# Performance work log

Measured on AMD Instinct MI355X. Metric: run time of the kernel, lower is better.

## Reference

```python
import jax, jax.numpy as jnp
import numpy as np

N = 100000
E = 1600000
F_IN, F_HID, F_OUT = 128, 32, 2


def setup_inputs() -> dict:
    key = jax.random.key(0)
    k1, k2, k3, k4 = jax.random.split(key, 4)
    x = jax.random.normal(k1, (N, F_IN), dtype=jnp.float32)
    edge_index = jax.random.randint(k2, (2, E), 0, N, dtype=jnp.int64)
    # Glorot-style init like torch_geometric GCNConv
    W1 = jax.random.normal(k3, (F_IN, F_HID), dtype=jnp.float32) * (1.0 / np.sqrt(F_IN))
    b1 = jnp.zeros((F_HID,), dtype=jnp.float32)
    W2 = jax.random.normal(k4, (F_HID, F_OUT), dtype=jnp.float32) * (1.0 / np.sqrt(F_HID))
    b2 = jnp.zeros((F_OUT,), dtype=jnp.float32)
    return {"x": x, "edge_index": edge_index, "W1": W1, "b1": b1, "W2": W2, "b2": b2}


def _gcn_conv(x, row, col, norm, W, b):
    # GCNConv: transform, then normalized aggregate (source -> target), then bias
    h = x @ W                                   # [N, F_out]
    msg = norm[:, None] * h[row]                # gather + scale, [E+N, F_out]
    out = jax.ops.segment_sum(msg, col, num_segments=N)  # scatter-add to targets
    return out + b


def reference(x, edge_index, W1, b1, W2, b2):
    # add self-loops (GCNConv default)
    loops = jnp.arange(N, dtype=edge_index.dtype)
    row = jnp.concatenate([edge_index[0], loops])
    col = jnp.concatenate([edge_index[1], loops])
    # symmetric normalization: deg^{-1/2}[row] * deg^{-1/2}[col], deg = in-degree w/ self-loops
    deg = jax.ops.segment_sum(jnp.ones_like(col, dtype=x.dtype), col, num_segments=N)
    dinv = jnp.where(deg > 0, jax.lax.rsqrt(deg), 0.0)
    norm = dinv[row] * dinv[col]                # [E+N]

    h = _gcn_conv(x, row, col, norm, W1, b1)
    h = jax.nn.relu(h)
    h = _gcn_conv(h, row, col, norm, W2, b2)
    return jax.nn.log_softmax(h, axis=1)
```

## Files before the change

kernel.cpp:

```cpp
#include <hip/hip_runtime.h>
#include <hip/hip_bf16.h>
#include <math.h>
#include <stdint.h>


#define GNN_N 100000
#define GNN_E 1600000
#define NBUCK 391
#define CAP 4608
#define CHB 4096

typedef float fx2 __attribute__((ext_vector_type(2)));
typedef short short8x __attribute__((ext_vector_type(8)));
typedef float f32x4 __attribute__((ext_vector_type(4)));

__device__ inline uint16_t bf16_bits(float f) {
    uint32_t u = __float_as_uint(f);
    return (uint16_t)((u + 0x7fffu + ((u >> 16) & 1u)) >> 16);
}

__global__ __launch_bounds__(256) void k_bucket(const int* __restrict__ row,
                                                const int* __restrict__ col,
                                                int* __restrict__ bucket_fill,
                                                uint32_t* __restrict__ slab, int e) {
    __shared__ int hist[NBUCK];
    __shared__ int base[NBUCK];
    const int tid = threadIdx.x;
    const int e0 = blockIdx.x * CHB;
    const int m = min(CHB, e - e0);
    const bool full = (m == CHB);

    for (int i = tid; i < NBUCK; i += 256) hist[i] = 0;

    int cc[16], rr[16], pp[16];
    if (full) {
        const int4* c4 = (const int4*)(col + e0);
        const int4* r4 = (const int4*)(row + e0);
        #pragma unroll
        for (int t = 0; t < 4; ++t) {
            int4 c = c4[tid + t * 256];
            int4 r = r4[tid + t * 256];
            cc[t * 4 + 0] = c.x; cc[t * 4 + 1] = c.y;
            cc[t * 4 + 2] = c.z; cc[t * 4 + 3] = c.w;
            rr[t * 4 + 0] = r.x; rr[t * 4 + 1] = r.y;
            rr[t * 4 + 2] = r.z; rr[t * 4 + 3] = r.w;
        }
        __syncthreads();
        #pragma unroll
        for (int t = 0; t < 16; ++t)
            pp[t] = atomicAdd(&hist[cc[t] >> 8], 1);
    } else {
        __syncthreads();
        #pragma unroll
        for (int t = 0; t < 16; ++t) {
            int i = tid + t * 256;
            if (i < m) {
                cc[t] = col[e0 + i];
                rr[t] = row[e0 + i];
                pp[t] = atomicAdd(&hist[cc[t] >> 8], 1);
            }
        }
    }
    __syncthreads();
    for (int i = tid; i < NBUCK; i += 256) {
        int bb = (i + blockIdx.x * 131) % NBUCK;
        base[bb] = atomicAdd(&bucket_fill[bb], hist[bb]);
    }
    __syncthreads();
    if (full) {
        #pragma unroll
        for (int t = 0; t < 16; ++t) {
            int b = cc[t] >> 8;
            int p = base[b] + pp[t];
            if (p < CAP)
                slab[(size_t)b * CAP + p] = ((uint32_t)rr[t] << 8) | (uint32_t)(cc[t] & 255);
        }
    } else {
        #pragma unroll
        for (int t = 0; t < 16; ++t) {
            int i = tid + t * 256;
            if (i < m) {
                int b = cc[t] >> 8;
                int p = base[b] + pp[t];
                if (p < CAP)
                    slab[(size_t)b * CAP + p] = ((uint32_t)rr[t] << 8) | (uint32_t)(cc[t] & 255);
            }
        }
    }
}

__global__ __launch_bounds__(512) void k_fine(const uint32_t* __restrict__ slab,
                                              const int* __restrict__ bucket_fill,
                                              int* __restrict__ sorted_row,
                                              int* __restrict__ offsets,
                                              float* __restrict__ dinv, int n) {
    __shared__ int hist[256];
    __shared__ int excl[256];
    __shared__ int wsum[4];
    __shared__ int s_gbase;
    __shared__ uint32_t stage[CAP];
    const int tid = threadIdx.x;
    const int b0 = blockIdx.x * 2;
    const int lane = tid & 63, wave = tid >> 6;

    if (blockIdx.x == gridDim.x - 1 && tid == 511) offsets[n] = GNN_E;

    if (tid < 64) {
        int s = 0;
        for (int i = tid; i < b0; i += 64) s += bucket_fill[i];
        #pragma unroll
        for (int m = 32; m >= 1; m >>= 1) s += __shfl_xor(s, m);
        if (tid == 0) s_gbase = s;
    }
    __syncthreads();
    int gbase = s_gbase;

    for (int pass = 0; pass < 2; ++pass) {
        const int b = b0 + pass;
        if (b >= NBUCK) break;
        const int nb = min(bucket_fill[b], CAP);
        const uint32_t* sl = slab + (size_t)b * CAP;

        if (tid < 256) hist[tid] = 0;
        __syncthreads();
        uint32_t uu[9];
        int pp[9];
        #pragma unroll
        for (int j = 0; j < 9; ++j) {
            int i = tid + j * 512;
            if (i < nb) {
                uint32_t u = sl[i];
                uu[j] = u;
                pp[j] = atomicAdd(&hist[u & 255u], 1);
            }
        }
        __syncthreads();
        int v = 0, inc = 0;
        if (tid < 256) {
            v = hist[tid];
            inc = v;
            #pragma unroll
            for (int d = 1; d < 64; d <<= 1) {
                int t = __shfl_up(inc, d);
                if (lane >= d) inc += t;
            }
            if (lane == 63) wsum[wave] = inc;
        }
        __syncthreads();
        if (tid == 0) {
            int a = 0;
            #pragma unroll
            for (int w = 0; w < 4; ++w) { int t = wsum[w]; wsum[w] = a; a += t; }
        }
        __syncthreads();
        if (tid < 256) {
            int ex = inc - v + wsum[wave];
            excl[tid] = ex;
            int c = b * 256 + tid;
            if (c < n) {
                offsets[c] = gbase + ex;
                dinv[c] = rsqrtf((float)(v + 1));
            }
        }
        __syncthreads();
        #pragma unroll
        for (int j = 0; j < 9; ++j) {
            int i = tid + j * 512;
            if (i < nb)
                stage[excl[uu[j] & 255u] + pp[j]] = uu[j] >> 8;
        }
        __syncthreads();
        for (int i = tid; i < nb; i += 512)
            sorted_row[gbase + i] = (int)stage[i];
        gbase += nb;
        __syncthreads();
    }
}

#define XPAD 136
__global__ __launch_bounds__(256) void k_matmul1(const float* __restrict__ x,
                                                 const float* __restrict__ W1,
                                                 const float* __restrict__ dinv,
                                                 uint32_t* __restrict__ h1q, int n) {
    __shared__ uint16_t xs[64 * XPAD];
    __shared__ uint16_t w1t[32 * XPAD];
    const int tid = threadIdx.x;
    const int nodeBase = blockIdx.x * 64;

    for (int i = tid; i < 4096; i += 256) {
        int k = i >> 5, c = i & 31;
        w1t[c * XPAD + k] = bf16_bits(W1[i]);
    }
    {
        const float4* x4 = (const float4*)x;
        for (int i = tid; i < 64 * 32; i += 256) {
            int node = i >> 5;
            int k4 = i & 31;
            float4 v = make_float4(0.f, 0.f, 0.f, 0.f);
            if (nodeBase + node < n)
                v = x4[(size_t)(nodeBase + node) * 32 + k4];
            int b = node * XPAD + k4 * 4;
            xs[b + 0] = bf16_bits(v.x); xs[b + 1] = bf16_bits(v.y);
            xs[b + 2] = bf16_bits(v.z); xs[b + 3] = bf16_bits(v.w);
        }
    }
    __syncthreads();

    const int wave = tid >> 6;
    const int lane = tid & 63;
    const int nn = lane & 15;
    const int quad = lane >> 4;
    f32x4 acc0 = {0.f, 0.f, 0.f, 0.f};
    f32x4 acc1 = {0.f, 0.f, 0.f, 0.f};
    const int xrow = (wave * 16 + nn) * XPAD;
    #pragma unroll
    for (int s = 0; s < 4; ++s) {
        const int kof = s * 32 + quad * 8;
        short8x bfrag = *(const short8x*)&xs[xrow + kof];
        short8x a0 = *(const short8x*)&w1t[nn * XPAD + kof];
        short8x a1 = *(const short8x*)&w1t[(16 + nn) * XPAD + kof];
        acc0 = __builtin_amdgcn_mfma_f32_16x16x32_bf16(a0, bfrag, acc0, 0, 0, 0);
        acc1 = __builtin_amdgcn_mfma_f32_16x16x32_bf16(a1, bfrag, acc1, 0, 0, 0);
    }
    const int gn = nodeBase + wave * 16 + nn;
    if (gn < n) {
        float d = dinv[gn];
        int w0 = 0, w1 = 0;
        w0 = __builtin_amdgcn_cvt_pk_fp8_f32(acc0[0] * d, acc0[1] * d, w0, false);
        w0 = __builtin_amdgcn_cvt_pk_fp8_f32(acc0[2] * d, acc0[3] * d, w0, true);
        w1 = __builtin_amdgcn_cvt_pk_fp8_f32(acc1[0] * d, acc1[1] * d, w1, false);
        w1 = __builtin_amdgcn_cvt_pk_fp8_f32(acc1[2] * d, acc1[3] * d, w1, true);
        h1q[(size_t)gn * 8 + quad] = (uint32_t)w0;
        h1q[(size_t)gn * 8 + 4 + quad] = (uint32_t)w1;
    }
}

__device__ inline void fp8x16_acc(float* a, uint4 u) {
    fx2 p;
    p = __builtin_amdgcn_cvt_pk_f32_fp8(u.x, false); a[0] += p.x;  a[1] += p.y;
    p = __builtin_amdgcn_cvt_pk_f32_fp8(u.x, true);  a[2] += p.x;  a[3] += p.y;
    p = __builtin_amdgcn_cvt_pk_f32_fp8(u.y, false); a[4] += p.x;  a[5] += p.y;
    p = __builtin_amdgcn_cvt_pk_f32_fp8(u.y, true);  a[6] += p.x;  a[7] += p.y;
    p = __builtin_amdgcn_cvt_pk_f32_fp8(u.z, false); a[8] += p.x;  a[9] += p.y;
    p = __builtin_amdgcn_cvt_pk_f32_fp8(u.z, true);  a[10] += p.x; a[11] += p.y;
    p = __builtin_amdgcn_cvt_pk_f32_fp8(u.w, false); a[12] += p.x; a[13] += p.y;
    p = __builtin_amdgcn_cvt_pk_f32_fp8(u.w, true);  a[14] += p.x; a[15] += p.y;
}

__global__ __launch_bounds__(256) void k_gather1(const int* __restrict__ offsets,
                                                 const int* __restrict__ sorted_row,
                                                 const uint32_t* __restrict__ h1q,
                                                 const float* __restrict__ dinv,
                                                 const float* __restrict__ b1,
                                                 const float* __restrict__ W2,
                                                 float* __restrict__ h2s, int n) {
    __shared__ float sb1[32];
    __shared__ float sW2[64];
    const int tid = threadIdx.x;
    if (tid < 32) sb1[tid] = b1[tid];
    else if (tid < 96) sW2[tid - 32] = W2[tid - 32];
    __syncthreads();

    const int l = tid & 1;
    const int node = blockIdx.x * 128 + (tid >> 1);
    if (node >= n) return;
    const uint4* h4 = (const uint4*)h1q;
    float acc[16], acc2[16];
    #pragma unroll
    for (int j = 0; j < 16; ++j) { acc[j] = 0.f; acc2[j] = 0.f; }
    fp8x16_acc(acc, h4[(size_t)node * 2 + l]);
    const int start = offsets[node];
    const int deg = offsets[node + 1] - start;
    const int* sr = sorted_row + start;
    int k = 0;
    for (; k + 8 <= deg; k += 8) {
        int r[8];
        uint4 u[8];
        #pragma unroll
        for (int t = 0; t < 8; ++t) r[t] = sr[k + t];
        #pragma unroll
        for (int t = 0; t < 8; ++t) u[t] = h4[(size_t)r[t] * 2 + l];
        #pragma unroll
        for (int t = 0; t < 8; ++t) fp8x16_acc((t & 1) ? acc2 : acc, u[t]);
    }
    for (; k + 2 <= deg; k += 2) {
        int ra = sr[k], rb = sr[k + 1];
        uint4 ua = h4[(size_t)ra * 2 + l];
        uint4 ub = h4[(size_t)rb * 2 + l];
        fp8x16_acc(acc, ua);
        fp8x16_acc(acc2, ub);
    }
    if (k < deg)
        fp8x16_acc(acc, h4[(size_t)sr[k] * 2 + l]);
    #pragma unroll
    for (int j = 0; j < 16; ++j) acc[j] += acc2[j];

    const float dc = dinv[node];
    const int f0 = l * 16;
    float s0 = 0.f, s1 = 0.f;
    #pragma unroll
    for (int j = 0; j < 16; ++j) {
        float a = fmaxf(dc * acc[j] + sb1[f0 + j], 0.f);
        s0 += a * sW2[(f0 + j) * 2];
        s1 += a * sW2[(f0 + j) * 2 + 1];
    }
    s0 += __shfl_xor(s0, 1);
    s1 += __shfl_xor(s1, 1);
    if (l == 0) ((float2*)h2s)[node] = make_float2(dc * s0, dc * s1);
}

__global__ __launch_bounds__(256) void k_gather2(const int* __restrict__ offsets,
                                                 const int* __restrict__ sorted_row,
                                                 const float* __restrict__ h2s,
                                                 const float* __restrict__ dinv,
                                                 const float* __restrict__ b2,
                                                 float* __restrict__ out, int n) {
    const int tid = threadIdx.x;
    const int l = tid & 3;
    const int node = blockIdx.x * 64 + (tid >> 2);
    if (node >= n) return;
    const float2* h2 = (const float2*)h2s;
    float sx = 0.f, sy = 0.f;
    if (l == 0) { float2 s = h2[node]; sx = s.x; sy = s.y; }
    const int start = offsets[node];
    const int deg = offsets[node + 1] - start;
    for (int k = l; k < deg; k += 4) {
        float2 v = h2[sorted_row[start + k]];
        sx += v.x; sy += v.y;
    }
    sx += __shfl_xor(sx, 1); sx += __shfl_xor(sx, 2);
    sy += __shfl_xor(sy, 1); sy += __shfl_xor(sy, 2);
    if (l == 0) {
        float d = dinv[node];
        float v0 = d * sx + b2[0];
        float v1 = d * sy + b2[1];
        float m = fmaxf(v0, v1);
        float lg = m + logf(expf(v0 - m) + expf(v1 - m));
        ((float2*)out)[node] = make_float2(v0 - lg, v1 - lg);
    }
}

extern "C" void kernel_launch(void* const* d_in, const int* in_sizes, int n_in,
                              void* d_out, int out_size, void* d_ws, size_t ws_size,
                              hipStream_t stream) {
    const float* x  = (const float*)d_in[0];
    const int*   ei = (const int*)d_in[1];
    const float* W1 = (const float*)d_in[2];
    const float* b1 = (const float*)d_in[3];
    const float* W2 = (const float*)d_in[4];
    const float* b2 = (const float*)d_in[5];
    float* out = (float*)d_out;
    char* ws = (char*)d_ws;

    const int N = GNN_N, E = GNN_E;
    const int* row = ei;
    const int* col = ei + GNN_E;

    float*    dinv        = (float*)    ws;
    int*      offsets     = (int*)     (ws + 4ull *  100000);
    int*      bucket_fill = (int*)     (ws + 4ull *  200512);
    int*      sorted_row  = (int*)     (ws + 4ull *  201024);
    float*    h2s         = (float*)   (ws + 4ull * 1801024);
    uint32_t* h1q         = (uint32_t*)(ws + 4ull * 2001024);
    uint32_t* slab        = (uint32_t*)(ws + 4ull * 2801024);

    hipMemsetAsync(bucket_fill, 0, NBUCK * sizeof(int), stream);

    k_bucket <<<(E + CHB - 1) / CHB, 256, 0, stream>>>(row, col, bucket_fill, slab, E);
    k_fine   <<<(NBUCK + 1) / 2, 512, 0, stream>>>(slab, bucket_fill, sorted_row, offsets, dinv, N);
    k_matmul1<<<(N + 63) / 64, 256, 0, stream>>>(x, W1, dinv, h1q, N);
    k_gather1<<<(N + 127) / 128, 256, 0, stream>>>(offsets, sorted_row, h1q, dinv, b1, W2, h2s, N);
    k_gather2<<<(N + 63) / 64, 256, 0, stream>>>(offsets, sorted_row, h2s, dinv, b2, out, N);
}
```

Baseline: 163.5 us.

## Fuse edge bucketing with first matmul and fold dinv scaling into fine sort

Merges the coarse bucketing kernel and the first-layer matmul into one launch, with blocks branching on their index, so the matmul no longer waits for the sort. The matmul now writes unscaled bf16 h1. The fine sort then rescales by dinv and converts to fp8 in place in the same buffer. Buckets shrink to 128 nodes, and sorted rows are written back into the slab in place. Offsets pack degree and start into one word, which removes the separate sorted_row array and the offsets[node+1] read. The risks are the extra bf16 write and read of h1, fixed per-bucket capacity, and degree clamped at 2047.

```diff
diff --git a/kernel.cpp b/kernel.cpp
--- a/kernel.cpp
+++ b/kernel.cpp
@@ -6,9 +6,11 @@
 
 #define GNN_N 100000
 #define GNN_E 1600000
-#define NBUCK 391
-#define CAP 4608
+#define NBUCK 782
+#define CAP 2560
 #define CHB 4096
+#define EB 391
+#define XPAD 136
 
 typedef float fx2 __attribute__((ext_vector_type(2)));
 typedef short short8x __attribute__((ext_vector_type(8)));
@@ -18,221 +20,232 @@
     uint32_t u = __float_as_uint(f);
     return (uint16_t)((u + 0x7fffu + ((u >> 16) & 1u)) >> 16);
 }
-
-__global__ __launch_bounds__(256) void k_bucket(const int* __restrict__ row,
-                                                const int* __restrict__ col,
-                                                int* __restrict__ bucket_fill,
-                                                uint32_t* __restrict__ slab, int e) {
-    __shared__ int hist[NBUCK];
-    __shared__ int base[NBUCK];
+__device__ inline uint32_t pack_bf2(float lo, float hi) {
+    return (uint32_t)bf16_bits(lo) | ((uint32_t)bf16_bits(hi) << 16);
+}
+
+__global__ __launch_bounds__(256) void k_fat(const int* __restrict__ row,
+                                             const int* __restrict__ col,
+                                             int* __restrict__ bucket_fill,
+                                             uint32_t* __restrict__ slab,
+                                             const float* __restrict__ x,
+                                             const float* __restrict__ W1,
+                                             uint32_t* __restrict__ h1,
+                                             int e, int n) {
+    __shared__ union {
+        struct { int hist[NBUCK]; int base[NBUCK]; } bk;
+        struct { uint16_t xs[64 * XPAD]; uint16_t w1t[32 * XPAD]; } mm;
+    } u;
     const int tid = threadIdx.x;
-    const int e0 = blockIdx.x * CHB;
-    const int m = min(CHB, e - e0);
-    const bool full = (m == CHB);
-
-    for (int i = tid; i < NBUCK; i += 256) hist[i] = 0;
-
-    int cc[16], rr[16], pp[16];
-    if (full) {
-        const int4* c4 = (const int4*)(col + e0);
-        const int4* r4 = (const int4*)(row + e0);
-        #pragma unroll
-        for (int t = 0; t < 4; ++t) {
-            int4 c = c4[tid + t * 256];
-            int4 r = r4[tid + t * 256];
-            cc[t * 4 + 0] = c.x; cc[t * 4 + 1] = c.y;
-            cc[t * 4 + 2] = c.z; cc[t * 4 + 3] = c.w;
-            rr[t * 4 + 0] = r.x; rr[t * 4 + 1] = r.y;
-            rr[t * 4 + 2] = r.z; rr[t * 4 + 3] = r.w;
+
+    if (blockIdx.x < EB) {
+        int* hist = u.bk.hist;
+        int* base = u.bk.base;
+        const int e0 = blockIdx.x * CHB;
+        const int m = min(CHB, e - e0);
+        const bool full = (m == CHB);
+
+        for (int i = tid; i < NBUCK; i += 256) hist[i] = 0;
+
+        int cc[16], rr[16], pp[16];
+        if (full) {
+            const int4* c4 = (const int4*)(col + e0);
+            const int4* r4 = (const int4*)(row + e0);
+            #pragma unroll
+            for (int t = 0; t < 4; ++t) {
+                int4 c = c4[tid + t * 256];
+                int4 r = r4[tid + t * 256];
+                cc[t * 4 + 0] = c.x; cc[t * 4 + 1] = c.y;
+                cc[t * 4 + 2] = c.z; cc[t * 4 + 3] = c.w;
+                rr[t * 4 + 0] = r.x; rr[t * 4 + 1] = r.y;
+                rr[t * 4 + 2] = r.z; rr[t * 4 + 3] = r.w;
+            }
+            __syncthreads();
+            #pragma unroll
+            for (int t = 0; t < 16; ++t)
+                pp[t] = atomicAdd(&hist[cc[t] >> 7], 1);
+        } else {
+            __syncthreads();
+            #pragma unroll
+            for (int t = 0; t < 16; ++t) {
+                int i = tid + t * 256;
+                if (i < m) {
+                    cc[t] = col[e0 + i];
+                    rr[t] = row[e0 + i];
+                    pp[t] = atomicAdd(&hist[cc[t] >> 7], 1);
+                }
+            }
         }
         __syncthreads();
-        #pragma unroll
-        for (int t = 0; t < 16; ++t)
-            pp[t] = atomicAdd(&hist[cc[t] >> 8], 1);
-    } else {
+        for (int i = tid; i < NBUCK; i += 256) {
+            int bb = (i + blockIdx.x * 131) % NBUCK;
+            base[bb] = atomicAdd(&bucket_fill[bb], hist[bb]);
+        }
         __syncthreads();
-        #pragma unroll
-        for (int t = 0; t < 16; ++t) {
-            int i = tid + t * 256;
-            if (i < m) {
-                cc[t] = col[e0 + i];
-                rr[t] = row[e0 + i];
-                pp[t] = atomicAdd(&hist[cc[t] >> 8], 1);
-            }
-        }
-    }
-    __syncthreads();
-    for (int i = tid; i < NBUCK; i += 256) {
-        int bb = (i + blockIdx.x * 131) % NBUCK;
-        base[bb] = atomicAdd(&bucket_fill[bb], hist[bb]);
-    }
-    __syncthreads();
-    if (full) {
-        #pragma unroll
-        for (int t = 0; t < 16; ++t) {
-            int b = cc[t] >> 8;
-            int p = base[b] + pp[t];
-            if (p < CAP)
-                slab[(size_t)b * CAP + p] = ((uint32_t)rr[t] << 8) | (uint32_t)(cc[t] & 255);
-        }
-    } else {
-        #pragma unroll
-        for (int t = 0; t < 16; ++t) {
-            int i = tid + t * 256;
-            if (i < m) {
-                int b = cc[t] >> 8;
+        if (full) {
+            #pragma unroll
+            for (int t = 0; t < 16; ++t) {
+                int b = cc[t] >> 7;
                 int p = base[b] + pp[t];
                 if (p < CAP)
-                    slab[(size_t)b * CAP + p] = ((uint32_t)rr[t] << 8) | (uint32_t)(cc[t] & 255);
-            }
-        }
-    }
-}
-
-__global__ __launch_bounds__(512) void k_fine(const uint32_t* __restrict__ slab,
+                    slab[(size_t)b * CAP + p] = ((uint32_t)rr[t] << 7) | (uint32_t)(cc[t] & 127);
+            }
+        } else {
+            #pragma unroll
+            for (int t = 0; t < 16; ++t) {
+                int i = tid + t * 256;
+                if (i < m) {
+                    int b = cc[t] >> 7;
+                    int p = base[b] + pp[t];
+                    if (p < CAP)
+                        slab[(size_t)b * CAP + p] = ((uint32_t)rr[t] << 7) | (uint32_t)(cc[t] & 127);
+                }
+            }
+        }
+    } else {
+        uint16_t* xs = u.mm.xs;
+        uint16_t* w1t = u.mm.w1t;
+        const int nodeBase = (blockIdx.x - EB) * 64;
+
+        for (int i = tid; i < 4096; i += 256) {
+            int k = i >> 5, c = i & 31;
+            w1t[c * XPAD + k] = bf16_bits(W1[i]);
+        }
+        {
+            const float4* x4 = (const float4*)x;
+            for (int i = tid; i < 64 * 32; i += 256) {
+                int node = i >> 5;
+                int k4 = i & 31;
+                float4 v = make_float4(0.f, 0.f, 0.f, 0.f);
+                if (nodeBase + node < n)
+                    v = x4[(size_t)(nodeBase + node) * 32 + k4];
+                int b = node * XPAD + k4 * 4;
+                xs[b + 0] = bf16_bits(v.x); xs[b + 1] = bf16_bits(v.y);
+                xs[b + 2] = bf16_bits(v.z); xs[b + 3] = bf16_bits(v.w);
+            }
+        }
+        __syncthreads();
+
+        const int wave = tid >> 6;
+        const int lane = tid & 63;
+        const int nn = lane & 15;
+        const int quad = lane >> 4;
+        f32x4 acc0 = {0.f, 0.f, 0.f, 0.f};
+        f32x4 acc1 = {0.f, 0.f, 0.f, 0.f};
+        const int xrow = (wave * 16 + nn) * XPAD;
+        #pragma unroll
+        for (int s = 0; s < 4; ++s) {
+            const int kof = s * 32 + quad * 8;
+            short8x bfrag = *(const short8x*)&xs[xrow + kof];
+            short8x a0 = *(const short8x*)&w1t[nn * XPAD + kof];
+            short8x a1 = *(const short8x*)&w1t[(16 + nn) * XPAD + kof];
+            acc0 = __builtin_amdgcn_mfma_f32_16x16x32_bf16(a0, bfrag, acc0, 0, 0, 0);
+            acc1 = __builtin_amdgcn_mfma_f32_16x16x32_bf16(a1, bfrag, acc1, 0, 0, 0);
+        }
+        const int gn = nodeBase + wave * 16 + nn;
+        if (gn < n) {
+            uint2* h1b2 = (uint2*)h1;
+            h1b2[(size_t)gn * 8 + quad] =
+                make_uint2(pack_bf2(acc0[0], acc0[1]), pack_bf2(acc0[2], acc0[3]));
+            h1b2[(size_t)gn * 8 + 4 + quad] =
+                make_uint2(pack_bf2(acc1[0], acc1[1]), pack_bf2(acc1[2], acc1[3]));
+        }
+    }
+}
+
+__global__ __launch_bounds__(512) void k_fine(uint32_t* __restrict__ slab,
                                               const int* __restrict__ bucket_fill,
-                                              int* __restrict__ sorted_row,
-                                              int* __restrict__ offsets,
+                                              uint32_t* __restrict__ h1,
+                                              uint32_t* __restrict__ offsets,
                                               float* __restrict__ dinv, int n) {
-    __shared__ int hist[256];
-    __shared__ int excl[256];
-    __shared__ int wsum[4];
-    __shared__ int s_gbase;
+    __shared__ int hist[128];
+    __shared__ int excl[128];
+    __shared__ int wsum[2];
     __shared__ uint32_t stage[CAP];
     const int tid = threadIdx.x;
-    const int b0 = blockIdx.x * 2;
+    const int b = blockIdx.x;
     const int lane = tid & 63, wave = tid >> 6;
 
-    if (blockIdx.x == gridDim.x - 1 && tid == 511) offsets[n] = GNN_E;
-
-    if (tid < 64) {
-        int s = 0;
-        for (int i = tid; i < b0; i += 64) s += bucket_fill[i];
-        #pragma unroll
-        for (int m = 32; m >= 1; m >>= 1) s += __shfl_xor(s, m);
-        if (tid == 0) s_gbase = s;
-    }
-    __syncthreads();
-    int gbase = s_gbase;
-
-    for (int pass = 0; pass < 2; ++pass) {
-        const int b = b0 + pass;
-        if (b >= NBUCK) break;
-        const int nb = min(bucket_fill[b], CAP);
-        const uint32_t* sl = slab + (size_t)b * CAP;
-
-        if (tid < 256) hist[tid] = 0;
-        __syncthreads();
-        uint32_t uu[9];
-        int pp[9];
-        #pragma unroll
-        for (int j = 0; j < 9; ++j) {
-            int i = tid + j * 512;
-            if (i < nb) {
-                uint32_t u = sl[i];
-                uu[j] = u;
-                pp[j] = atomicAdd(&hist[u & 255u], 1);
-            }
-        }
-        __syncthreads();
-        int v = 0, inc = 0;
-        if (tid < 256) {
-            v = hist[tid];
-            inc = v;
-            #pragma unroll
-            for (int d = 1; d < 64; d <<= 1) {
-                int t = __shfl_up(inc, d);
-                if (lane >= d) inc += t;
-            }
-            if (lane == 63) wsum[wave] = inc;
-        }
-        __syncthreads();
-        if (tid == 0) {
-            int a = 0;
-            #pragma unroll
-            for (int w = 0; w < 4; ++w) { int t = wsum[w]; wsum[w] = a; a += t; }
-        }
-        __syncthreads();
-        if (tid < 256) {
-            int ex = inc - v + wsum[wave];
-            excl[tid] = ex;
-            int c = b * 256 + tid;
-            if (c < n) {
-                offsets[c] = gbase + ex;
-                dinv[c] = rsqrtf((float)(v + 1));
-            }
-        }
-        __syncthreads();
-        #pragma unroll
-        for (int j = 0; j < 9; ++j) {
-            int i = tid + j * 512;
-            if (i < nb)
-                stage[excl[uu[j] & 255u] + pp[j]] = uu[j] >> 8;
-        }
-        __syncthreads();
-        for (int i = tid; i < nb; i += 512)
-            sorted_row[gbase + i] = (int)stage[i];
-        gbase += nb;
-        __syncthreads();
-    }
-}
-
-#define XPAD 136
-__global__ __launch_bounds__(256) void k_matmul1(const float* __restrict__ x,
-                                                 const float* __restrict__ W1,
-                                                 const float* __restrict__ dinv,
-                                                 uint32_t* __restrict__ h1q, int n) {
-    __shared__ uint16_t xs[64 * XPAD];
-    __shared__ uint16_t w1t[32 * XPAD];
-    const int tid = threadIdx.x;
-    const int nodeBase = blockIdx.x * 64;
-
-    for (int i = tid; i < 4096; i += 256) {
-        int k = i >> 5, c = i & 31;
-        w1t[c * XPAD + k] = bf16_bits(W1[i]);
-    }
-    {
-        const float4* x4 = (const float4*)x;
-        for (int i = tid; i < 64 * 32; i += 256) {
-            int node = i >> 5;
-            int k4 = i & 31;
-            float4 v = make_float4(0.f, 0.f, 0.f, 0.f);
-            if (nodeBase + node < n)
-                v = x4[(size_t)(nodeBase + node) * 32 + k4];
-            int b = node * XPAD + k4 * 4;
-            xs[b + 0] = bf16_bits(v.x); xs[b + 1] = bf16_bits(v.y);
-            xs[b + 2] = bf16_bits(v.z); xs[b + 3] = bf16_bits(v.w);
-        }
-    }
-    __syncthreads();
-
-    const int wave = tid >> 6;
-    const int lane = tid & 63;
-    const int nn = lane & 15;
-    const int quad = lane >> 4;
-    f32x4 acc0 = {0.f, 0.f, 0.f, 0.f};
-    f32x4 acc1 = {0.f, 0.f, 0.f, 0.f};
-    const int xrow = (wave * 16 + nn) * XPAD;
-    #pragma unroll
-    for (int s = 0; s < 4; ++s) {
-        const int kof = s * 32 + quad * 8;
-        short8x bfrag = *(const short8x*)&xs[xrow + kof];
-        short8x a0 = *(const short8x*)&w1t[nn * XPAD + kof];
-        short8x a1 = *(const short8x*)&w1t[(16 + nn) * XPAD + kof];
-        acc0 = __builtin_amdgcn_mfma_f32_16x16x32_bf16(a0, bfrag, acc0, 0, 0, 0);
-        acc1 = __builtin_amdgcn_mfma_f32_16x16x32_bf16(a1, bfrag, acc1, 0, 0, 0);
-    }
-    const int gn = nodeBase + wave * 16 + nn;
-    if (gn < n) {
-        float d = dinv[gn];
-        int w0 = 0, w1 = 0;
-        w0 = __builtin_amdgcn_cvt_pk_fp8_f32(acc0[0] * d, acc0[1] * d, w0, false);
-        w0 = __builtin_amdgcn_cvt_pk_fp8_f32(acc0[2] * d, acc0[3] * d, w0, true);
-        w1 = __builtin_amdgcn_cvt_pk_fp8_f32(acc1[0] * d, acc1[1] * d, w1, false);
-        w1 = __builtin_amdgcn_cvt_pk_fp8_f32(acc1[2] * d, acc1[3] * d, w1, true);
-        h1q[(size_t)gn * 8 + quad] = (uint32_t)w0;
-        h1q[(size_t)gn * 8 + 4 + quad] = (uint32_t)w1;
-    }
+    if (tid < 128) hist[tid] = 0;
+    __syncthreads();
+    const int nb = min(bucket_fill[b], CAP);
+    uint32_t* sl = slab + (size_t)b * CAP;
+
+    uint32_t uu[5];
+    int pp[5];
+    #pragma unroll
+    for (int j = 0; j < 5; ++j) {
+        int i = tid + j * 512;
+        if (i < nb) {
+            uint32_t u = sl[i];
+            uu[j] = u;
+            pp[j] = atomicAdd(&hist[u & 127u], 1);
+        }
+    }
+    __syncthreads();
+    int v = 0, inc = 0;
+    if (tid < 128) {
+        v = hist[tid];
+        inc = v;
+        #pragma unroll
+        for (int d = 1; d < 64; d <<= 1) {
+            int t = __shfl_up(inc, d);
+            if (lane >= d) inc += t;
+        }
+        if (lane == 63) wsum[wave] = inc;
+    }
+    __syncthreads();
+    if (tid == 0) { int t0 = wsum[0]; wsum[0] = 0; wsum[1] = t0; }
+    __syncthreads();
+    if (tid < 128) {
+        int ex = inc - v + wsum[wave];
+        excl[tid] = ex;
+        int c = b * 128 + tid;
+        if (c < n) {
+            offsets[c] = ((uint32_t)min(v, 2047) << 21) | (uint32_t)(b * CAP + ex);
+            dinv[c] = rsqrtf((float)(v + 1));
+        }
+    }
+    __syncthreads();
+    #pragma unroll
+    for (int j = 0; j < 5; ++j) {
+        int i = tid + j * 512;
+        if (i < nb)
+            stage[excl[uu[j] & 127u] + pp[j]] = uu[j] >> 7;
+    }
+    const uint2* h1b2 = (const uint2*)h1;
+    uint2 ru[2]; float rdc[2]; int rc[2], rq[2]; bool rvld[2];
+    #pragma unroll
+    for (int it = 0; it < 2; ++it) {
+        int d = tid + it * 512;
+        int node = d >> 3;
+        rq[it] = d & 7;
+        int c = b * 128 + node;
+        rc[it] = c;
+        rvld[it] = (c < n);
+        if (rvld[it]) {
+            rdc[it] = rsqrtf((float)(hist[node] + 1));
+            ru[it] = h1b2[(size_t)c * 8 + rq[it]];
+        }
+    }
+    __syncthreads();
+    #pragma unroll
+    for (int it = 0; it < 2; ++it) {
+        if (rvld[it]) {
+            float dc = rdc[it];
+            uint2 u2 = ru[it];
+            float a0 = __uint_as_float(u2.x << 16) * dc;
+            float a1 = __uint_as_float(u2.x & 0xffff0000u) * dc;
+            float a2 = __uint_as_float(u2.y << 16) * dc;
+            float a3 = __uint_as_float(u2.y & 0xffff0000u) * dc;
+            int w = 0;
+            w = __builtin_amdgcn_cvt_pk_fp8_f32(a0, a1, w, false);
+            w = __builtin_amdgcn_cvt_pk_fp8_f32(a2, a3, w, true);
+            h1[(size_t)rc[it] * 16 + rq[it]] = (uint32_t)w;
+        }
+    }
+    for (int i = tid; i < nb; i += 512)
+        sl[i] = stage[i];
 }
 
 __device__ inline void fp8x16_acc(float* a, uint4 u) {
@@ -247,9 +260,9 @@
     p = __builtin_amdgcn_cvt_pk_f32_fp8(u.w, true);  a[14] += p.x; a[15] += p.y;
 }
 
-__global__ __launch_bounds__(256) void k_gather1(const int* __restrict__ offsets,
-                                                 const int* __restrict__ sorted_row,
-                                                 const uint32_t* __restrict__ h1q,
+__global__ __launch_bounds__(256) void k_gather1(const uint32_t* __restrict__ offsets,
+                                                 const uint32_t* __restrict__ sorted,
+                                                 const uint32_t* __restrict__ h1,
                                                  const float* __restrict__ dinv,
                                                  const float* __restrict__ b1,
                                                  const float* __restrict__ W2,
@@ -264,34 +277,35 @@
     const int l = tid & 1;
     const int node = blockIdx.x * 128 + (tid >> 1);
     if (node >= n) return;
-    const uint4* h4 = (const uint4*)h1q;
+    const uint4* h4 = (const uint4*)h1;
     float acc[16], acc2[16];
     #pragma unroll
     for (int j = 0; j < 16; ++j) { acc[j] = 0.f; acc2[j] = 0.f; }
-    fp8x16_acc(acc, h4[(size_t)node * 2 + l]);
-    const int start = offsets[node];
-    const int deg = offsets[node + 1] - start;
-    const int* sr = sorted_row + start;
+    fp8x16_acc(acc, h4[(size_t)node * 4 + l]);
+    const uint32_t ow = offsets[node];
+    const int start = (int)(ow & 0x1FFFFFu);
+    const int deg = (int)(ow >> 21);
+    const uint32_t* sr = sorted + start;
     int k = 0;
     for (; k + 8 <= deg; k += 8) {
         int r[8];
         uint4 u[8];
         #pragma unroll
-        for (int t = 0; t < 8; ++t) r[t] = sr[k + t];
-        #pragma unroll
-        for (int t = 0; t < 8; ++t) u[t] = h4[(size_t)r[t] * 2 + l];
+        for (int t = 0; t < 8; ++t) r[t] = (int)sr[k + t];
+        #pragma unroll
+        for (int t = 0; t < 8; ++t) u[t] = h4[(size_t)r[t] * 4 + l];
         #pragma unroll
         for (int t = 0; t < 8; ++t) fp8x16_acc((t & 1) ? acc2 : acc, u[t]);
     }
     for (; k + 2 <= deg; k += 2) {
-        int ra = sr[k], rb = sr[k + 1];
-        uint4 ua = h4[(size_t)ra * 2 + l];
-        uint4 ub = h4[(size_t)rb * 2 + l];
+        int ra = (int)sr[k], rb = (int)sr[k + 1];
+        uint4 ua = h4[(size_t)ra * 4 + l];
+        uint4 ub = h4[(size_t)rb * 4 + l];
         fp8x16_acc(acc, ua);
         fp8x16_acc(acc2, ub);
     }
     if (k < deg)
-        fp8x16_acc(acc, h4[(size_t)sr[k] * 2 + l]);
+        fp8x16_acc(acc, h4[(size_t)sr[k] * 4 + l]);
     #pragma unroll
     for (int j = 0; j < 16; ++j) acc[j] += acc2[j];
 
@@ -309,8 +323,8 @@
     if (l == 0) ((float2*)h2s)[node] = make_float2(dc * s0, dc * s1);
 }
 
-__global__ __launch_bounds__(256) void k_gather2(const int* __restrict__ offsets,
-                                                 const int* __restrict__ sorted_row,
+__global__ __launch_bounds__(256) void k_gather2(const uint32_t* __restrict__ offsets,
+                                                 const uint32_t* __restrict__ sorted,
                                                  const float* __restrict__ h2s,
                                                  const float* __restrict__ dinv,
                                                  const float* __restrict__ b2,
@@ -322,10 +336,11 @@
     const float2* h2 = (const float2*)h2s;
     float sx = 0.f, sy = 0.f;
     if (l == 0) { float2 s = h2[node]; sx = s.x; sy = s.y; }
-    const int start = offsets[node];
-    const int deg = offsets[node + 1] - start;
+    const uint32_t ow = offsets[node];
+    const int start = (int)(ow & 0x1FFFFFu);
+    const int deg = (int)(ow >> 21);
     for (int k = l; k < deg; k += 4) {
-        float2 v = h2[sorted_row[start + k]];
+        float2 v = h2[sorted[start + k]];
         sx += v.x; sy += v.y;
     }
     sx += __shfl_xor(sx, 1); sx += __shfl_xor(sx, 2);
@@ -357,18 +372,17 @@
     const int* col = ei + GNN_E;
 
     float*    dinv        = (float*)    ws;
-    int*      offsets     = (int*)     (ws + 4ull *  100000);
-    int*      bucket_fill = (int*)     (ws + 4ull *  200512);
-    int*      sorted_row  = (int*)     (ws + 4ull *  201024);
-    float*    h2s         = (float*)   (ws + 4ull * 1801024);
-    uint32_t* h1q         = (uint32_t*)(ws + 4ull * 2001024);
-    uint32_t* slab        = (uint32_t*)(ws + 4ull * 2801024);
-
-    hipMemsetAsync(bucket_fill, 0, NBUCK * sizeof(int), stream);
-
-    k_bucket <<<(E + CHB - 1) / CHB, 256, 0, stream>>>(row, col, bucket_fill, slab, E);
-    k_fine   <<<(NBUCK + 1) / 2, 512, 0, stream>>>(slab, bucket_fill, sorted_row, offsets, dinv, N);
-    k_matmul1<<<(N + 63) / 64, 256, 0, stream>>>(x, W1, dinv, h1q, N);
-    k_gather1<<<(N + 127) / 128, 256, 0, stream>>>(offsets, sorted_row, h1q, dinv, b1, W2, h2s, N);
-    k_gather2<<<(N + 63) / 64, 256, 0, stream>>>(offsets, sorted_row, h2s, dinv, b2, out, N);
-}
+    uint32_t* offsets     = (uint32_t*)(ws + 4ull *  100000);
+    int*      bucket_fill = (int*)     (ws + 4ull *  200000);
+    float*    h2s         = (float*)   (ws + 4ull *  201024);
+    uint32_t* h1          = (uint32_t*)(ws + 4ull *  401024);
+    uint32_t* slab        = (uint32_t*)(ws + 4ull * 2001024);
+
+    hipMemsetAsync(bucket_fill, 0, 1024 * sizeof(int), stream);
+
+    const int MB = (N + 63) / 64;
+    k_fat    <<<EB + MB, 256, 0, stream>>>(row, col, bucket_fill, slab, x, W1, h1, E, N);
+    k_fine   <<<NBUCK, 512, 0, stream>>>(slab, bucket_fill, h1, offsets, dinv, N);
+    k_gather1<<<(N + 127) / 128, 256, 0, stream>>>(offsets, slab, h1, dinv, b1, W2, h2s, N);
+    k_gather2<<<(N + 63) / 64, 256, 0, stream>>>(offsets, slab, h2s, dinv, b2, out, N);
+}
```

Result: slower. 171.4 us (+4.8%).
